# Kernel optimization log

Measured on AMD Instinct MI355X. Metric: run time of the kernel, lower is better.

Reference implementation:

```python
import jax, jax.numpy as jnp
import numpy as np

N_HEADS = 8
TOP_K = 100


def setup_inputs() -> dict:
    key = jax.random.key(0)
    ks = jax.random.split(key, 12)
    B, S, H, U = 16, 2048, 1024, 512
    s = 0.02
    return {
        "query": jax.random.normal(ks[0], (B, H), jnp.float32),
        "values": jax.random.normal(ks[1], (B, S, H), jnp.float32),
        # stacked per-head Bahdanau params (8 heads)
        "W1": jax.random.normal(ks[2], (N_HEADS, H, U), jnp.float32) * s,
        "b1": jnp.zeros((N_HEADS, U), jnp.float32),
        "W2": jax.random.normal(ks[3], (N_HEADS, H, U), jnp.float32) * s,
        "b2": jnp.zeros((N_HEADS, U), jnp.float32),
        "Vw": jax.random.normal(ks[4], (N_HEADS, U), jnp.float32) * s,
        "Vb": jnp.zeros((N_HEADS,), jnp.float32),
        # head-mixing linear W: nbr_heads -> 1
        "Ww": jax.random.normal(ks[5], (N_HEADS,), jnp.float32) * s,
        "Wb": jnp.zeros((), jnp.float32),
    }


def reference(query, values, W1, b1, W2, b2, Vw, Vb, Ww, Wb):
    # per-head additive attention scores, vectorized over the 8 heads
    # values: [B,S,H], query: [B,H]
    hid = jnp.tanh(
        jnp.einsum('bsh,nhu->nbsu', values, W1) + b1[:, None, None, :]
        + jnp.einsum('bh,nhu->nbu', query, W2)[:, :, None, :] + b2[:, None, None, :]
    )  # [N,B,S,U]
    scores = jnp.einsum('nbsu,nu->bsn', hid, Vw) + Vb  # [B,S,N] == concat of 8 head scores
    score = jnp.einsum('bsn,n->bs', scores, Ww) + Wb   # [B,S]

    # topk over sequence dim, then zero all non-topk positions:
    # torch: score = -(score.scatter(1, top_pos, 0) - score)
    _, top_pos = jax.lax.top_k(score, TOP_K)           # [B,K]
    bidx = jnp.arange(score.shape[0])[:, None]
    sc0 = score.at[bidx, top_pos].set(0.0)
    masked = (score - sc0)[..., None]                  # [B,S,1]: topk vals kept, 0 else

    # custom sigmoid 'softmax' normalized over the BATCH dim (dim 0), as in source
    w = jax.nn.sigmoid(masked)
    w = w / w.sum(0)                                   # [B,S,1]
    context = (w * values).sum(1)                      # [B,H]
    return context, w, masked
```

## Files before the change

kernel.cpp:

```cpp
#include <hip/hip_runtime.h>
#include <hip/hip_bf16.h>

#define B_ 16
#define S_ 2048
#define H_ 1024
#define U_ 512
#define NH 8
#define TOPK 100

#define M_ (B_*S_)
#define NC (NH*U_)

typedef int i32x4 __attribute__((ext_vector_type(4)));

__device__ __forceinline__ float fast_tanh(float x) {
    float e = __expf(2.f * x);
    return (e - 1.f) / (e + 1.f);
}

__device__ __forceinline__ void gl16i(const signed char* g, signed char* l) {
    __builtin_amdgcn_global_load_lds(
        (const __attribute__((address_space(1))) void*)g,
        (__attribute__((address_space(3))) void*)l, 16, 0, 0);
}

__global__ void cvtA(const float* __restrict__ v,
                     signed char* __restrict__ h8,
                     signed char* __restrict__ l8,
                     float* __restrict__ sa) {
    int row = blockIdx.x * 4 + (threadIdx.x >> 6);
    int l = threadIdx.x & 63;
    const float4* r4 = (const float4*)(v + (size_t)row * 1024);
    float4 x[4];
    float mx = 0.f;
    #pragma unroll
    for (int c = 0; c < 4; ++c) {
        x[c] = r4[l * 4 + c];
        mx = fmaxf(mx, fmaxf(fmaxf(fabsf(x[c].x), fabsf(x[c].y)),
                             fmaxf(fabsf(x[c].z), fabsf(x[c].w))));
    }
    #pragma unroll
    for (int d = 1; d < 64; d <<= 1) mx = fmaxf(mx, __shfl_xor(mx, d));
    float inv = 127.f / mx;
    int wh[4], wl[4];
    #pragma unroll
    for (int c = 0; c < 4; ++c) {
        float xs[4] = {x[c].x, x[c].y, x[c].z, x[c].w};
        unsigned ph = 0, pl = 0;
        #pragma unroll
        for (int j = 0; j < 4; ++j) {
            float y = xs[j] * inv;
            float hf = rintf(y);
            float lf = rintf((y - hf) * 128.f);
            ph |= ((unsigned)((int)hf) & 0xffu) << (8 * j);
            pl |= ((unsigned)((int)lf) & 0xffu) << (8 * j);
        }
        wh[c] = (int)ph; wl[c] = (int)pl;
    }
    *(int4*)(h8 + (size_t)row * 1024 + l * 16) = make_int4(wh[0], wh[1], wh[2], wh[3]);
    *(int4*)(l8 + (size_t)row * 1024 + l * 16) = make_int4(wl[0], wl[1], wl[2], wl[3]);
    if (l == 0) sa[row] = mx / 127.f;
}

__global__ void colmax_init(float* __restrict__ cm) {
    cm[blockIdx.x * 256 + threadIdx.x] = 0.f;
}
__global__ void colmax_kernel(const float* __restrict__ W1, float* __restrict__ cm) {
    int n = blockIdx.x, h0 = blockIdx.y * 64, u = threadIdx.x;
    const float* p = W1 + ((size_t)n * H_ + h0) * U_ + u;
    float mx = 0.f;
    #pragma unroll 8
    for (int h = 0; h < 64; ++h) mx = fmaxf(mx, fabsf(p[(size_t)h * U_]));
    atomicMax((unsigned*)(cm + n * U_ + u), __float_as_uint(mx));
}
__global__ void colmax_fin(const float* __restrict__ cm,
                           float* __restrict__ sbq, float* __restrict__ sbinv) {
    int c = blockIdx.x * 256 + threadIdx.x;
    float mx = cm[c];
    sbq[c] = mx / 127.f;
    sbinv[c] = 127.f / mx;
}

__global__ void cvtB8(const float* __restrict__ W1,
                      const float* __restrict__ sbinv,
                      signed char* __restrict__ bh) {
    __shared__ float t[64][65];
    int n = blockIdx.x, h0 = blockIdx.y * 64, u0 = blockIdx.z * 64;
    int tid = threadIdx.x;
    int ul = tid & 63;
    #pragma unroll
    for (int i = 0; i < 16; ++i) {
        int hl = i * 4 + (tid >> 6);
        t[hl][ul] = W1[((size_t)n * H_ + h0 + hl) * U_ + u0 + ul];
    }
    __syncthreads();
    #pragma unroll
    for (int i = 0; i < 16; ++i) {
        int ulw = i * 4 + (tid >> 6);
        int hlw = tid & 63;
        float q = t[hlw][ulw] * sbinv[n * 512 + u0 + ulw];
        size_t o = ((size_t)(n * 512 + u0 + ulw)) * 1024 + h0 + hlw;
        bh[o] = (signed char)(int)rintf(q);
    }
}

__global__ void qb_kernel(const float* __restrict__ query,
                          const float* __restrict__ W2,
                          const float* __restrict__ b1,
                          const float* __restrict__ b2,
                          float* __restrict__ qb) {
    int n = blockIdx.x >> 4;
    int b = blockIdx.x & 15;
    __shared__ float q[H_];
    int tid = threadIdx.x;
    q[tid]       = query[b * H_ + tid];
    q[tid + 512] = query[b * H_ + tid + 512];
    __syncthreads();
    const float* w2 = W2 + (size_t)n * H_ * U_ + tid;
    float acc = 0.f;
    #pragma unroll 4
    for (int h = 0; h < H_; ++h) acc += q[h] * w2[(size_t)h * U_];
    acc += b1[n * U_ + tid] + b2[n * U_ + tid];
    qb[(n * B_ + b) * U_ + tid] = acc;
}

#define NT 16
#define SWZ(d) ((d) ^ ((((d) >> 7) & 3) << 4))
#define K0B(tt) ((tt) * 64)
#define STAGE_A(tt, j) gl16i(Ah8 + (size_t)(rowBase + (j)*128 + rT) * 1024 + K0B(tt) + cTb, \
                             lds + ((tt)&3)*32768 + (j)*8192 + tid*16)
#define STAGE_B(tt, j) gl16i(Bh8 + (size_t)(colBase + (j)*128 + rT) * 1024 + K0B(tt) + cTb, \
                             lds + ((tt)&3)*32768 + 16384 + (j)*8192 + tid*16)

__global__ __launch_bounds__(512, 1) void gemm8i(
        const signed char* __restrict__ Ah8,
        const signed char* __restrict__ Bh8,
        const float* __restrict__ sa, const float* __restrict__ sbq,
        const float* __restrict__ qb, const float* __restrict__ Vw,
        const float* __restrict__ Ww, float* __restrict__ partial) {
    __shared__ signed char lds[131072];
    const int tid = threadIdx.x;
    const int lane = tid & 63;
    const int wid = tid >> 6;
    const int wm = wid >> 2, wn = wid & 3;
    int bid = blockIdx.x;
    int swz = (bid & 7) * 256 + (bid >> 3);
    int mIdx = swz & 127, nIdx = swz >> 7;
    int rowBase = mIdx * 256, colBase = nIdx * 256;

    int d0 = tid * 16;
    int d0s = SWZ(d0);
    int rT  = d0s >> 6;
    int cTb = d0s & 63;

    const int l15 = lane & 15, l4 = lane >> 4;
    int offA[8], offB[4];
    #pragma unroll
    for (int m = 0; m < 8; ++m)
        offA[m] = SWZ((wm * 128 + m * 16 + l15) * 64 + l4 * 16);
    #pragma unroll
    for (int n = 0; n < 4; ++n)
        offB[n] = 16384 + SWZ((wn * 64 + n * 16 + l15) * 64 + l4 * 16);

    i32x4 acc[8][4];
    #pragma unroll
    for (int m = 0; m < 8; ++m)
        #pragma unroll
        for (int n = 0; n < 4; ++n) acc[m][n] = (i32x4){0, 0, 0, 0};

    #pragma unroll
    for (int tt = 0; tt < 3; ++tt) {
        STAGE_A(tt, 0); STAGE_A(tt, 1);
        STAGE_B(tt, 0); STAGE_B(tt, 1);
    }
    asm volatile("s_waitcnt vmcnt(8)" ::: "memory");
    __builtin_amdgcn_s_barrier();

    #pragma unroll 1
    for (int t = 0; t < NT; ++t) {
        __builtin_amdgcn_sched_barrier(0);
        if (t <= NT - 4) {
            STAGE_A(t + 3, 0); STAGE_A(t + 3, 1);
            STAGE_B(t + 3, 0); STAGE_B(t + 3, 1);
        }
        const signed char* slot = lds + (t & 3) * 32768;
        i32x4 bf[4], af[8];
        #pragma unroll
        for (int n = 0; n < 4; ++n) bf[n] = *(const i32x4*)(slot + offB[n]);
        #pragma unroll
        for (int m = 0; m < 8; ++m) af[m] = *(const i32x4*)(slot + offA[m]);
        #pragma unroll
        for (int m = 0; m < 8; ++m)
            #pragma unroll
            for (int n = 0; n < 4; ++n)
                acc[m][n] = __builtin_amdgcn_mfma_i32_16x16x64_i8(af[m], bf[n], acc[m][n], 0, 0, 0);
        asm volatile("s_waitcnt lgkmcnt(0)" ::: "memory");
        if (t <= NT - 4)      asm volatile("s_waitcnt vmcnt(8)" ::: "memory");
        else if (t == NT - 3) asm volatile("s_waitcnt vmcnt(4)" ::: "memory");
        else if (t == NT - 2) asm volatile("s_waitcnt vmcnt(0)" ::: "memory");
        __builtin_amdgcn_s_barrier();
    }

    __syncthreads();
    int hd = colBase >> 9;
    int b = rowBase >> 11;
    float wwn = Ww[hd];
    float qv[4], vw[4], sbv[4];
    #pragma unroll
    for (int n = 0; n < 4; ++n) {
        int col = colBase + wn * 64 + n * 16 + l15;
        int u = col & 511;
        qv[n] = qb[((size_t)hd * B_ + b) * U_ + u];
        vw[n] = Vw[hd * U_ + u] * wwn;
        sbv[n] = sbq[col];
    }
    float* red = (float*)lds;
    #pragma unroll
    for (int m = 0; m < 8; ++m) {
        float sav[4];
        #pragma unroll
        for (int r = 0; r < 4; ++r)
            sav[r] = sa[rowBase + wm * 128 + m * 16 + l4 * 4 + r];
        #pragma unroll
        for (int r = 0; r < 4; ++r) {
            float p = 0.f;
            #pragma unroll
            for (int n = 0; n < 4; ++n)
                p += vw[n] * fast_tanh((float)acc[m][n][r] * sav[r] * sbv[n] + qv[n]);
            p += __shfl_xor(p, 1);
            p += __shfl_xor(p, 2);
            p += __shfl_xor(p, 4);
            p += __shfl_xor(p, 8);
            if (l15 == 0)
                red[wn * 256 + wm * 128 + m * 16 + l4 * 4 + r] = p;
        }
    }
    __syncthreads();
    if (tid < 256) {
        float s = red[tid] + red[256 + tid] + red[512 + tid] + red[768 + tid];
        partial[(size_t)nIdx * M_ + rowBase + tid] = s;
    }
}

__global__ __launch_bounds__(256, 2) void gemm_score(
        const float* __restrict__ values,
        const float* __restrict__ W1,
        const float* __restrict__ qb,
        const float* __restrict__ Vw,
        const float* __restrict__ Ww,
        float* __restrict__ partial) {
    __shared__ float As[16][128 + 4];
    __shared__ float Bs[16][128 + 4];
    int tid = threadIdx.x;
    int tx = tid & 15, ty = tid >> 4;
    int rowBase = blockIdx.x * 128;
    int colBase = blockIdx.y * 128;
    int n = colBase >> 9;
    int u0 = colBase & 511;
    int b = rowBase >> 11;
    float acc[8][8];
    #pragma unroll
    for (int i = 0; i < 8; ++i)
        #pragma unroll
        for (int j = 0; j < 8; ++j) acc[i][j] = 0.f;
    const float* Ag = values + (size_t)rowBase * H_;
    const float* Bg = W1 + (size_t)n * H_ * U_ + u0;
    for (int k0 = 0; k0 < H_; k0 += 16) {
        #pragma unroll
        for (int r = 0; r < 2; ++r) {
            int idx = tid + r * 256;
            int arow = idx >> 2, aqc = idx & 3;
            float4 v = *(const float4*)(Ag + (size_t)arow * H_ + k0 + aqc * 4);
            As[aqc * 4 + 0][arow] = v.x;
            As[aqc * 4 + 1][arow] = v.y;
            As[aqc * 4 + 2][arow] = v.z;
            As[aqc * 4 + 3][arow] = v.w;
        }
        #pragma unroll
        for (int r = 0; r < 2; ++r) {
            int idx = tid + r * 256;
            int bk = idx >> 5, bqc = idx & 31;
            float4 v = *(const float4*)(Bg + (size_t)(k0 + bk) * U_ + bqc * 4);
            *(float4*)&Bs[bk][bqc * 4] = v;
        }
        __syncthreads();
        #pragma unroll
        for (int k = 0; k < 16; ++k) {
            float4 a0 = *(const float4*)&As[k][ty * 8];
            float4 a1 = *(const float4*)&As[k][ty * 8 + 4];
            float4 b0 = *(const float4*)&Bs[k][tx * 8];
            float4 b1v = *(const float4*)&Bs[k][tx * 8 + 4];
            float av[8] = {a0.x, a0.y, a0.z, a0.w, a1.x, a1.y, a1.z, a1.w};
            float bv[8] = {b0.x, b0.y, b0.z, b0.w, b1v.x, b1v.y, b1v.z, b1v.w};
            #pragma unroll
            for (int i = 0; i < 8; ++i)
                #pragma unroll
                for (int j = 0; j < 8; ++j)
                    acc[i][j] = fmaf(av[i], bv[j], acc[i][j]);
        }
        __syncthreads();
    }
    float qbv[8], vwv[8];
    #pragma unroll
    for (int j = 0; j < 8; ++j) {
        int u = u0 + tx * 8 + j;
        qbv[j] = qb[(n * B_ + b) * U_ + u];
        vwv[j] = Vw[n * U_ + u];
    }
    float wwn = Ww[n];
    #pragma unroll
    for (int i = 0; i < 8; ++i) {
        float p = 0.f;
        #pragma unroll
        for (int j = 0; j < 8; ++j)
            p += vwv[j] * fast_tanh(acc[i][j] + qbv[j]);
        p += __shfl_xor(p, 1);
        p += __shfl_xor(p, 2);
        p += __shfl_xor(p, 4);
        p += __shfl_xor(p, 8);
        if (tx == 0)
            partial[(size_t)blockIdx.y * M_ + rowBase + ty * 8 + i] = wwn * p;
    }
}

__global__ __launch_bounds__(1024) void topk_kernel(
        const float* __restrict__ partial, int nparts,
        const float* __restrict__ Vb,
        const float* __restrict__ Ww,
        const float* __restrict__ Wb,
        float* __restrict__ out_masked,
        float* __restrict__ w_un) {
    __shared__ float sc[S_];
    __shared__ float srt[S_];
    __shared__ int cnt_gt;
    int b = blockIdx.x;
    int tid = threadIdx.x;
    float cst = Wb[0];
    #pragma unroll
    for (int n2 = 0; n2 < NH; ++n2) cst += Ww[n2] * Vb[n2];
    for (int s = tid; s < S_; s += 1024) {
        float v = cst;
        for (int ct = 0; ct < nparts; ++ct)
            v += partial[(size_t)ct * M_ + b * S_ + s];
        sc[s] = v; srt[s] = v;
    }
    if (tid == 0) cnt_gt = 0;
    __syncthreads();
    for (int k = 2; k <= S_; k <<= 1) {
        for (int j = k >> 1; j >= 1; j >>= 1) {
            int i = ((tid & ~(j - 1)) << 1) | (tid & (j - 1));
            int p = i | j;
            float a = srt[i], c2 = srt[p];
            if (((i & k) == 0) ? (a > c2) : (a < c2)) { srt[i] = c2; srt[p] = a; }
            __syncthreads();
        }
    }
    float T = srt[S_ - TOPK];
    int c = 0;
    for (int s = tid; s < S_; s += 1024) c += (sc[s] > T);
    atomicAdd(&cnt_gt, c);
    __syncthreads();
    int need_eq = TOPK - cnt_gt;
    for (int s = tid; s < S_; s += 1024) {
        float v = sc[s];
        bool sel = (v > T);
        if (v == T) {
            int rank = 0;
            for (int t2 = 0; t2 < s; ++t2) rank += (sc[t2] == T);
            sel = (rank < need_eq);
        }
        float m = sel ? v : 0.f;
        out_masked[b * S_ + s] = m;
        w_un[b * S_ + s] = 1.f / (1.f + __expf(-m));
    }
}

__global__ void norm_w(const float* __restrict__ w_un, float* __restrict__ out_w) {
    int s = blockIdx.x * blockDim.x + threadIdx.x;
    float d = 0.f;
    #pragma unroll
    for (int b = 0; b < B_; ++b) d += w_un[b * S_ + s];
    float inv = 1.f / d;
    #pragma unroll
    for (int b = 0; b < B_; ++b) out_w[b * S_ + s] = w_un[b * S_ + s] * inv;
}

__global__ void ctx_partial_i8(const signed char* __restrict__ h8,
                               const signed char* __restrict__ l8,
                               const float* __restrict__ sa,
                               const float* __restrict__ w,
                               float* __restrict__ pctx) {
    int bb = blockIdx.x;
    int h = blockIdx.y * 256 + threadIdx.x;
    int s0 = blockIdx.z * 256;
    __shared__ float ws[256], wsl[256];
    {
        int s = threadIdx.x;
        float wv = w[bb * S_ + s0 + s];
        float sv = sa[bb * S_ + s0 + s];
        ws[s] = wv * sv;
        wsl[s] = wv * sv * (1.f / 128.f);
    }
    __syncthreads();
    const signed char* hp = h8 + (size_t)(bb * S_ + s0) * H_ + h;
    const signed char* lp = l8 + (size_t)(bb * S_ + s0) * H_ + h;
    float acc = 0.f;
    #pragma unroll 4
    for (int s = 0; s < 256; ++s) {
        acc += ws[s] * (float)hp[(size_t)s * H_];
        acc += wsl[s] * (float)lp[(size_t)s * H_];
    }
    pctx[((size_t)blockIdx.z * B_ + bb) * H_ + h] = acc;
}

__global__ void ctx_partial_f32(const float* __restrict__ values,
                                const float* __restrict__ w,
                                float* __restrict__ pctx) {
    int bb = blockIdx.x;
    int h = blockIdx.y * 256 + threadIdx.x;
    int s0 = blockIdx.z * 256;
    __shared__ float wrow[256];
    wrow[threadIdx.x] = w[bb * S_ + s0 + threadIdx.x];
    __syncthreads();
    const float* vp = values + (size_t)(bb * S_ + s0) * H_ + h;
    float acc = 0.f;
    #pragma unroll 4
    for (int s = 0; s < 256; ++s) acc += wrow[s] * vp[(size_t)s * H_];
    pctx[((size_t)blockIdx.z * B_ + bb) * H_ + h] = acc;
}

__global__ void ctx_reduce(const float* __restrict__ pctx,
                           float* __restrict__ out_ctx) {
    int i = blockIdx.x * blockDim.x + threadIdx.x;
    float s = 0.f;
    #pragma unroll
    for (int z = 0; z < 8; ++z) s += pctx[(size_t)z * B_ * H_ + i];
    out_ctx[i] = s;
}

extern "C" void kernel_launch(void* const* d_in, const int* in_sizes, int n_in,
                              void* d_out, int out_size, void* d_ws, size_t ws_size,
                              hipStream_t stream) {
    const float* query = (const float*)d_in[0];
    const float* values = (const float*)d_in[1];
    const float* W1 = (const float*)d_in[2];
    const float* b1 = (const float*)d_in[3];
    const float* W2 = (const float*)d_in[4];
    const float* b2 = (const float*)d_in[5];
    const float* Vw = (const float*)d_in[6];
    const float* Vb = (const float*)d_in[7];
    const float* Ww = (const float*)d_in[8];
    const float* Wb = (const float*)d_in[9];

    float* ws = (float*)d_ws;
    float* qb      = ws;
    float* partial = qb + 65536;
    float* score   = partial + 1048576;
    float* w_un    = score + 32768;
    float* pctx    = w_un + 32768;
    float* sa      = pctx + 131072;
    float* sbq     = sa + 32768;
    float* sbinv   = sbq + 4096;
    float* colmax  = sbinv + 4096;
    signed char* Ah8 = (signed char*)(colmax + 4096);
    signed char* Al8 = Ah8 + (size_t)M_ * H_;
    signed char* Bh8 = Al8 + (size_t)M_ * H_;
    size_t needed = (size_t)((char*)(Bh8 + (size_t)NC * H_) - (char*)d_ws);

    float* out_ctx    = (float*)d_out;
    float* out_w      = out_ctx + 16384;
    float* out_masked = out_w + 32768;

    qb_kernel<<<dim3(NH * B_), 512, 0, stream>>>(query, W2, b1, b2, qb);
    if (ws_size >= needed) {
        cvtA<<<dim3(8192), 256, 0, stream>>>(values, Ah8, Al8, sa);
        colmax_init<<<dim3(16), 256, 0, stream>>>(colmax);
        colmax_kernel<<<dim3(NH, 16), 512, 0, stream>>>(W1, colmax);
        colmax_fin<<<dim3(16), 256, 0, stream>>>(colmax, sbq, sbinv);
        cvtB8<<<dim3(NH, 16, 8), 256, 0, stream>>>(W1, sbinv, Bh8);
        gemm8i<<<dim3(2048), 512, 0, stream>>>(Ah8, Bh8, sa, sbq,
                                               qb, Vw, Ww, partial);
        topk_kernel<<<16, 1024, 0, stream>>>(partial, 16, Vb, Ww, Wb, out_masked, w_un);
        norm_w<<<8, 256, 0, stream>>>(w_un, out_w);
        ctx_partial_i8<<<dim3(16, 4, 8), 256, 0, stream>>>(Ah8, Al8, sa, out_w, pctx);
    } else {
        gemm_score<<<dim3(256, 32), 256, 0, stream>>>(values, W1, qb, Vw, Ww, partial);
        topk_kernel<<<16, 1024, 0, stream>>>(partial, 32, Vb, Ww, Wb, out_masked, w_un);
        norm_w<<<8, 256, 0, stream>>>(w_un, out_w);
        ctx_partial_f32<<<dim3(16, 4, 8), 256, 0, stream>>>(values, out_w, pctx);
    }
    ctx_reduce<<<64, 256, 0, stream>>>(pctx, out_ctx);
}
```

Measured before the change: 473.0 us.

## Drop low-byte residual of values quantization and split qb projection across blocks

The int8 conversion of values no longer writes a second residual byte plane, and the context reduction reads only the high int8 plane. This removes 32 MB of writes and reads, at the cost of lower precision in the context output. The qb projection is split into 128 blocks over h-chunks plus a small reduce kernel, replacing the previous 128 serial-over-H blocks. The colmax init and finalize kernels are replaced by a memset and inline scale computation, which saves launches.

```diff
diff --git a/kernel.cpp b/kernel.cpp
--- a/kernel.cpp
+++ b/kernel.cpp
@@ -26,7 +26,6 @@
 
 __global__ void cvtA(const float* __restrict__ v,
                      signed char* __restrict__ h8,
-                     signed char* __restrict__ l8,
                      float* __restrict__ sa) {
     int row = blockIdx.x * 4 + (threadIdx.x >> 6);
     int l = threadIdx.x & 63;
@@ -42,29 +41,22 @@
     #pragma unroll
     for (int d = 1; d < 64; d <<= 1) mx = fmaxf(mx, __shfl_xor(mx, d));
     float inv = 127.f / mx;
-    int wh[4], wl[4];
+    int wh[4];
     #pragma unroll
     for (int c = 0; c < 4; ++c) {
         float xs[4] = {x[c].x, x[c].y, x[c].z, x[c].w};
-        unsigned ph = 0, pl = 0;
+        unsigned ph = 0;
         #pragma unroll
         for (int j = 0; j < 4; ++j) {
-            float y = xs[j] * inv;
-            float hf = rintf(y);
-            float lf = rintf((y - hf) * 128.f);
+            float hf = rintf(xs[j] * inv);
             ph |= ((unsigned)((int)hf) & 0xffu) << (8 * j);
-            pl |= ((unsigned)((int)lf) & 0xffu) << (8 * j);
-        }
-        wh[c] = (int)ph; wl[c] = (int)pl;
+        }
+        wh[c] = (int)ph;
     }
     *(int4*)(h8 + (size_t)row * 1024 + l * 16) = make_int4(wh[0], wh[1], wh[2], wh[3]);
-    *(int4*)(l8 + (size_t)row * 1024 + l * 16) = make_int4(wl[0], wl[1], wl[2], wl[3]);
     if (l == 0) sa[row] = mx / 127.f;
 }
 
-__global__ void colmax_init(float* __restrict__ cm) {
-    cm[blockIdx.x * 256 + threadIdx.x] = 0.f;
-}
 __global__ void colmax_kernel(const float* __restrict__ W1, float* __restrict__ cm) {
     int n = blockIdx.x, h0 = blockIdx.y * 64, u = threadIdx.x;
     const float* p = W1 + ((size_t)n * H_ + h0) * U_ + u;
@@ -73,16 +65,9 @@
     for (int h = 0; h < 64; ++h) mx = fmaxf(mx, fabsf(p[(size_t)h * U_]));
     atomicMax((unsigned*)(cm + n * U_ + u), __float_as_uint(mx));
 }
-__global__ void colmax_fin(const float* __restrict__ cm,
-                           float* __restrict__ sbq, float* __restrict__ sbinv) {
-    int c = blockIdx.x * 256 + threadIdx.x;
-    float mx = cm[c];
-    sbq[c] = mx / 127.f;
-    sbinv[c] = 127.f / mx;
-}
 
 __global__ void cvtB8(const float* __restrict__ W1,
-                      const float* __restrict__ sbinv,
+                      const float* __restrict__ cm,
                       signed char* __restrict__ bh) {
     __shared__ float t[64][65];
     int n = blockIdx.x, h0 = blockIdx.y * 64, u0 = blockIdx.z * 64;
@@ -98,30 +83,51 @@
     for (int i = 0; i < 16; ++i) {
         int ulw = i * 4 + (tid >> 6);
         int hlw = tid & 63;
-        float q = t[hlw][ulw] * sbinv[n * 512 + u0 + ulw];
+        float q = t[hlw][ulw] * (127.f / cm[n * 512 + u0 + ulw]);
         size_t o = ((size_t)(n * 512 + u0 + ulw)) * 1024 + h0 + hlw;
         bh[o] = (signed char)(int)rintf(q);
     }
 }
 
-__global__ void qb_kernel(const float* __restrict__ query,
-                          const float* __restrict__ W2,
+__global__ void qbp_kernel(const float* __restrict__ query,
+                           const float* __restrict__ W2,
+                           float* __restrict__ qbp) {
+    int n = blockIdx.x, hc = blockIdx.y;
+    int u = threadIdx.x;
+    int h0 = hc * 64;
+    __shared__ float q[16][64];
+    #pragma unroll
+    for (int k = 0; k < 2; ++k) {
+        int idx = threadIdx.x + k * 512;
+        q[idx >> 6][idx & 63] = query[(idx >> 6) * H_ + h0 + (idx & 63)];
+    }
+    __syncthreads();
+    float acc[16];
+    #pragma unroll
+    for (int b = 0; b < 16; ++b) acc[b] = 0.f;
+    const float* w2 = W2 + ((size_t)n * H_ + h0) * U_ + u;
+    #pragma unroll 4
+    for (int hh = 0; hh < 64; ++hh) {
+        float wv = w2[(size_t)hh * U_];
+        #pragma unroll
+        for (int b = 0; b < 16; ++b) acc[b] = fmaf(q[b][hh], wv, acc[b]);
+    }
+    float* dst = qbp + ((size_t)hc * NH + n) * 16 * U_ + u;
+    #pragma unroll
+    for (int b = 0; b < 16; ++b) dst[(size_t)b * U_] = acc[b];
+}
+
+__global__ void qb_reduce(const float* __restrict__ qbp,
                           const float* __restrict__ b1,
                           const float* __restrict__ b2,
                           float* __restrict__ qb) {
-    int n = blockIdx.x >> 4;
-    int b = blockIdx.x & 15;
-    __shared__ float q[H_];
-    int tid = threadIdx.x;
-    q[tid]       = query[b * H_ + tid];
-    q[tid + 512] = query[b * H_ + tid + 512];
-    __syncthreads();
-    const float* w2 = W2 + (size_t)n * H_ * U_ + tid;
-    float acc = 0.f;
-    #pragma unroll 4
-    for (int h = 0; h < H_; ++h) acc += q[h] * w2[(size_t)h * U_];
-    acc += b1[n * U_ + tid] + b2[n * U_ + tid];
-    qb[(n * B_ + b) * U_ + tid] = acc;
+    int i = blockIdx.x * 256 + threadIdx.x;
+    int n = i >> 13;
+    int u = i & 511;
+    float s = b1[n * U_ + u] + b2[n * U_ + u];
+    #pragma unroll
+    for (int hc = 0; hc < 16; ++hc) s += qbp[(size_t)hc * 65536 + i];
+    qb[i] = s;
 }
 
 #define NT 16
@@ -135,7 +141,7 @@
 __global__ __launch_bounds__(512, 1) void gemm8i(
         const signed char* __restrict__ Ah8,
         const signed char* __restrict__ Bh8,
-        const float* __restrict__ sa, const float* __restrict__ sbq,
+        const float* __restrict__ sa, const float* __restrict__ cm,
         const float* __restrict__ qb, const float* __restrict__ Vw,
         const float* __restrict__ Ww, float* __restrict__ partial) {
     __shared__ signed char lds[131072];
@@ -212,7 +218,7 @@
         int u = col & 511;
         qv[n] = qb[((size_t)hd * B_ + b) * U_ + u];
         vw[n] = Vw[hd * U_ + u] * wwn;
-        sbv[n] = sbq[col];
+        sbv[n] = cm[col] * (1.f / 127.f);
     }
     float* red = (float*)lds;
     #pragma unroll
@@ -385,31 +391,24 @@
     for (int b = 0; b < B_; ++b) out_w[b * S_ + s] = w_un[b * S_ + s] * inv;
 }
 
-__global__ void ctx_partial_i8(const signed char* __restrict__ h8,
-                               const signed char* __restrict__ l8,
+__global__ void ctx_partial_h8(const signed char* __restrict__ h8,
                                const float* __restrict__ sa,
                                const float* __restrict__ w,
                                float* __restrict__ pctx) {
     int bb = blockIdx.x;
     int h = blockIdx.y * 256 + threadIdx.x;
     int s0 = blockIdx.z * 256;
-    __shared__ float ws[256], wsl[256];
+    __shared__ float ws[256];
     {
         int s = threadIdx.x;
-        float wv = w[bb * S_ + s0 + s];
-        float sv = sa[bb * S_ + s0 + s];
-        ws[s] = wv * sv;
-        wsl[s] = wv * sv * (1.f / 128.f);
+        ws[s] = w[bb * S_ + s0 + s] * sa[bb * S_ + s0 + s];
     }
     __syncthreads();
     const signed char* hp = h8 + (size_t)(bb * S_ + s0) * H_ + h;
-    const signed char* lp = l8 + (size_t)(bb * S_ + s0) * H_ + h;
     float acc = 0.f;
     #pragma unroll 4
-    for (int s = 0; s < 256; ++s) {
+    for (int s = 0; s < 256; ++s)
         acc += ws[s] * (float)hp[(size_t)s * H_];
-        acc += wsl[s] * (float)lp[(size_t)s * H_];
-    }
     pctx[((size_t)blockIdx.z * B_ + bb) * H_ + h] = acc;
 }
 
@@ -454,35 +453,32 @@
 
     float* ws = (float*)d_ws;
     float* qb      = ws;
-    float* partial = qb + 65536;
-    float* score   = partial + 1048576;
-    float* w_un    = score + 32768;
+    float* qbp     = qb + 65536;
+    float* partial = qbp + 1048576;
+    float* w_un    = partial + 1048576;
     float* pctx    = w_un + 32768;
     float* sa      = pctx + 131072;
-    float* sbq     = sa + 32768;
-    float* sbinv   = sbq + 4096;
-    float* colmax  = sbinv + 4096;
+    float* colmax  = sa + 32768;
     signed char* Ah8 = (signed char*)(colmax + 4096);
-    signed char* Al8 = Ah8 + (size_t)M_ * H_;
-    signed char* Bh8 = Al8 + (size_t)M_ * H_;
+    signed char* Bh8 = Ah8 + (size_t)M_ * H_;
     size_t needed = (size_t)((char*)(Bh8 + (size_t)NC * H_) - (char*)d_ws);
 
     float* out_ctx    = (float*)d_out;
     float* out_w      = out_ctx + 16384;
     float* out_masked = out_w + 32768;
 
-    qb_kernel<<<dim3(NH * B_), 512, 0, stream>>>(query, W2, b1, b2, qb);
+    qbp_kernel<<<dim3(NH, 16), 512, 0, stream>>>(query, W2, qbp);
+    qb_reduce<<<dim3(256), 256, 0, stream>>>(qbp, b1, b2, qb);
     if (ws_size >= needed) {
-        cvtA<<<dim3(8192), 256, 0, stream>>>(values, Ah8, Al8, sa);
-        colmax_init<<<dim3(16), 256, 0, stream>>>(colmax);
+        cvtA<<<dim3(8192), 256, 0, stream>>>(values, Ah8, sa);
+        hipMemsetAsync(colmax, 0, NC * sizeof(float), stream);
         colmax_kernel<<<dim3(NH, 16), 512, 0, stream>>>(W1, colmax);
-        colmax_fin<<<dim3(16), 256, 0, stream>>>(colmax, sbq, sbinv);
-        cvtB8<<<dim3(NH, 16, 8), 256, 0, stream>>>(W1, sbinv, Bh8);
-        gemm8i<<<dim3(2048), 512, 0, stream>>>(Ah8, Bh8, sa, sbq,
+        cvtB8<<<dim3(NH, 16, 8), 256, 0, stream>>>(W1, colmax, Bh8);
+        gemm8i<<<dim3(2048), 512, 0, stream>>>(Ah8, Bh8, sa, colmax,
                                                qb, Vw, Ww, partial);
         topk_kernel<<<16, 1024, 0, stream>>>(partial, 16, Vb, Ww, Wb, out_masked, w_un);
         norm_w<<<8, 256, 0, stream>>>(w_un, out_w);
-        ctx_partial_i8<<<dim3(16, 4, 8), 256, 0, stream>>>(Ah8, Al8, sa, out_w, pctx);
+        ctx_partial_h8<<<dim3(16, 4, 8), 256, 0, stream>>>(Ah8, sa, out_w, pctx);
     } else {
         gemm_score<<<dim3(256, 32), 256, 0, stream>>>(values, W1, qb, Vw, Ww, partial);
         topk_kernel<<<16, 1024, 0, stream>>>(partial, 32, Vb, Ww, Wb, out_masked, w_un);
```

Result: faster. 400.5 us (-15.3%).
